# Kernel tuning notes

Measured on AMD Instinct MI355X. Metric: run time of the kernel, lower is better.

The kernel has to match this reference:

```python
import jax, jax.numpy as jnp
import numpy as np

N_NODES, N_EDGES, D_IN, N_GRAPHS = 20000, 320000, 256, 32
H1, C1, H2, C2 = 4, 128, 4, 64


def setup_inputs() -> dict:
    key = jax.random.key(0)
    ks = jax.random.split(key, 24)
    g = lambda k, shape, fan: jax.random.normal(k, shape, jnp.float32) * (1.0 / np.sqrt(fan))
    inp = {
        'x': jax.random.normal(ks[0], (N_NODES, D_IN), jnp.float32),
        'edge_index': jax.random.randint(ks[1], (2, N_EDGES), 0, N_NODES, jnp.int32),
        'batch': jnp.sort(jax.random.randint(ks[2], (N_NODES,), 0, N_GRAPHS, jnp.int32)),
        'edge_attr': jax.random.normal(ks[3], (N_EDGES, 1), jnp.float32),
        # GATConv 1: lin [D_IN, H1*C1], att_src/dst/edge [H1,C1], lin_edge [1,H1*C1], bias [H1*C1]
        'W1': g(ks[4], (D_IN, H1 * C1), D_IN),
        'as1': g(ks[5], (H1, C1), C1),
        'ad1': g(ks[6], (H1, C1), C1),
        'We1': g(ks[7], (1, H1 * C1), 1),
        'ae1': g(ks[8], (H1, C1), C1),
        'b1': jnp.zeros((H1 * C1,), jnp.float32),
        'g1': jnp.ones((H1 * C1,), jnp.float32),
        'be1': jnp.zeros((H1 * C1,), jnp.float32),
        # GATConv 2 (concat=False -> out 64)
        'W2': g(ks[9], (H1 * C1, H2 * C2), H1 * C1),
        'as2': g(ks[10], (H2, C2), C2),
        'ad2': g(ks[11], (H2, C2), C2),
        'We2': g(ks[12], (1, H2 * C2), 1),
        'ae2': g(ks[13], (H2, C2), C2),
        'b2': jnp.zeros((C2,), jnp.float32),
        'g2': jnp.ones((C2,), jnp.float32),
        'be2': jnp.zeros((C2,), jnp.float32),
        'fw1': g(ks[14], (C2, 32), C2),
        'fb1': jnp.zeros((32,), jnp.float32),
        'fw2': g(ks[15], (32, 1), 32),
        'fb2': jnp.zeros((1,), jnp.float32),
    }
    return inp


def _gat(x, src, dst, ea, W, a_s, a_d, We, a_e, bias, H, C, concat, n):
    h = (x @ W).reshape(n, H, C)                         # [N,H,C]
    al_s = jnp.einsum('nhc,hc->nh', h, a_s)              # [N,H]
    al_d = jnp.einsum('nhc,hc->nh', h, a_d)
    e = (ea @ We).reshape(-1, H, C)                      # [E',H,C]
    al_e = jnp.einsum('ehc,hc->eh', e, a_e)
    logits = jax.nn.leaky_relu(al_s[src] + al_d[dst] + al_e, 0.2)  # [E',H]
    m = jax.ops.segment_max(logits, dst, num_segments=n)
    m = jnp.where(jnp.isfinite(m), m, 0.0)
    p = jnp.exp(logits - m[dst])
    denom = jax.ops.segment_sum(p, dst, num_segments=n)
    alpha = p / (denom[dst] + 1e-16)                     # segment softmax
    out = jax.ops.segment_sum(h[src] * alpha[:, :, None], dst, num_segments=n)
    out = out.reshape(n, H * C) if concat else out.mean(axis=1)
    return out + bias


def _bn(x, gamma, beta):
    mu = x.mean(axis=0)
    var = x.var(axis=0)
    return gamma * (x - mu) * jax.lax.rsqrt(var + 1e-5) + beta


def reference(x, edge_index, batch, edge_attr, W1, as1, ad1, We1, ae1, b1, g1, be1,
              W2, as2, ad2, We2, ae2, b2, g2, be2, fw1, fb1, fw2, fb2):
    n = x.shape[0]
    loop = jnp.arange(n, dtype=edge_index.dtype)
    src = jnp.concatenate([edge_index[0], loop])
    dst = jnp.concatenate([edge_index[1], loop])
    # self-loop edge_attr filled with mean (PyG fill_value='mean')
    ea = jnp.concatenate([edge_attr, jnp.broadcast_to(edge_attr.mean(axis=0), (n, edge_attr.shape[1]))])

    h = _gat(x, src, dst, ea, W1, as1, ad1, We1, ae1, b1, H1, C1, True, n)
    h = jax.nn.elu(_bn(h, g1, be1))
    h = _gat(h, src, dst, ea, W2, as2, ad2, We2, ae2, b2, H2, C2, False, n)
    h = jax.nn.elu(_bn(h, g2, be2))

    sums = jax.ops.segment_sum(h, batch, num_segments=N_GRAPHS)
    cnt = jax.ops.segment_sum(jnp.ones((n,), h.dtype), batch, num_segments=N_GRAPHS)
    pooled = sums / jnp.maximum(cnt, 1.0)[:, None]       # global_mean_pool
    # dropout is identity in eval mode
    out = jax.nn.elu(pooled @ fw1 + fb1) @ fw2 + fb2
    return out
```

## Files before the change

kernel.cpp:

```cpp
#include <hip/hip_runtime.h>
#include <hip/hip_bf16.h>

#define N_NODES  20000
#define MPAD     20096
#define N_EDGES  320000
#define N_EP     (N_EDGES + N_NODES)
#define D_IN     256
#define N_GRAPHS 32
#define HH1 4
#define CC1 128
#define HH2 4
#define CC2 64
#define MAXDEG   128

#define XB_OFF      0ull
#define HB1_OFF     10289152ull
#define AGG1_OFF    30867456ull
#define HB2_OFF     51445760ull
#define OUT2_OFF    61734912ull
#define EAF_OFF     66854912ull
#define W1BT_OFF    68134912ull
#define W2BT_OFF    68397056ull
#define CSR_OFF     68659200ull
#define ROWPTR_OFF  71379200ull
#define GSTART_OFF  71459264ull
#define SMALL_OFF   71459520ull
#define SBUF_OFF    71485120ull
#define EAP_OFF     71485184ull
#define PMU1_OFF    72772608ull
#define PM21_OFF    73296896ull
#define PMU2_OFF    73821184ull
#define PM22_OFF    73886720ull
#define A1_OFF      73952256ull
#define B1_OFF      73954304ull
#define A2_OFF      73956352ull
#define B2_OFF      73956608ull
#define EAACC_OFF   73956864ull
#define DEG_OFF     74600000ull
#define CURS_OFF    74680000ull
#define FLAGZ_OFF   74760000ull
#define PP_OFF      74760128ull
#define ALS1_OFF    74825664ull
#define ALD1_OFF    75147200ull
#define ALS2_OFF    75468736ull
#define ALD2_OFF    75790272ull
#define ZERO0_START DEG_OFF
#define ZERO0_SIZE  1511808ull

#define S_AS1 0
#define S_AD1 512
#define S_WE1 1024
#define S_AE1 1536
#define S_G1  2048
#define S_BE1 2560
#define S_AS2 3072
#define S_AD2 3328
#define S_WE2 3584
#define S_AE2 3840
#define S_G2  4096
#define S_BE2 4160
#define S_FW1 4224
#define S_FB1 6272
#define S_FW2 6304
#define S_FB2 6336

typedef __attribute__((ext_vector_type(8))) short bf8_t;
typedef __attribute__((ext_vector_type(4))) float f4_t;

__global__ void detect_dtype(const unsigned short* __restrict__ xr, int* __restrict__ flag) {
    int i = blockIdx.x * blockDim.x + threadIdx.x;
    unsigned short u = xr[i];
    if ((u & 0x7F80) == 0x7F80) atomicOr(flag, 1);
}

__device__ __forceinline__ float loadF(const void* p, int i, int fp32) {
    return fp32 ? ((const float*)p)[i]
                : __bfloat162float(((const __hip_bfloat16*)p)[i]);
}

#define PB_XB  5024
#define PB_EAF 313
#define PB_W   512
#define PB_SM  16
#define PREP_BLOCKS (PB_XB + PB_EAF + 2 * PB_W + PB_SM + 1)
__global__ __launch_bounds__(256) void prep(
        const int* __restrict__ flag,
        const void* x, const void* ea, const void* W1, const void* W2,
        const void* as1, const void* ad1, const void* We1, const void* ae1,
        const void* g1, const void* be1, const void* as2, const void* ad2,
        const void* We2, const void* ae2, const void* g2, const void* be2,
        const void* fw1, const void* fb1, const void* fw2, const void* fb2,
        __hip_bfloat16* __restrict__ xb, float* __restrict__ eaf, float* __restrict__ eap,
        __hip_bfloat16* __restrict__ W1bt, __hip_bfloat16* __restrict__ W2bt,
        float* __restrict__ smalls, float* __restrict__ sbuf) {
    __shared__ float sh[256];
    int b = blockIdx.x, t = threadIdx.x;
    int fp32 = flag[0];
    if (b < PB_XB) {
        int base = (b * 256 + t) * 4;
        __hip_bfloat16 tmp[4];
#pragma unroll
        for (int j = 0; j < 4; ++j) {
            int i = base + j;
            float v = (i < N_NODES * D_IN) ? loadF(x, i, fp32) : 0.f;
            tmp[j] = __float2bfloat16(v);
        }
        *(uint2*)&xb[base] = *(uint2*)tmp;
        return;
    }
    b -= PB_XB;
    if (b < PB_EAF) {
        int base = (b * 256 + t) * 4;
        float s = 0.f;
#pragma unroll
        for (int j = 0; j < 4; ++j) {
            int i = base + j;
            if (i < N_EDGES) { float v = loadF(ea, i, fp32); eaf[i] = v; s += v; }
        }
        sh[t] = s;
        __syncthreads();
        for (int st = 128; st; st >>= 1) {
            if (t < st) sh[t] += sh[t + st];
            __syncthreads();
        }
        if (t == 0) eap[b] = sh[0];
        return;
    }
    b -= PB_EAF;
    if (b < PB_W) {
        int i = b * 256 + t;
        int k = i >> 9, n = i & 511;
        W1bt[(size_t)n * 256 + k] = __float2bfloat16(loadF(W1, i, fp32));
        return;
    }
    b -= PB_W;
    if (b < PB_W) {
        int i = b * 256 + t;
        int k = i >> 8, n = i & 255;
        W2bt[(size_t)n * 512 + k] = __float2bfloat16(loadF(W2, i, fp32));
        return;
    }
    b -= PB_W;
    if (b < PB_SM) {
        const void* srcs[16] = {as1, ad1, We1, ae1, g1, be1, as2, ad2, We2, ae2, g2, be2, fw1, fb1, fw2, fb2};
        const int cnts[16] = {512, 512, 512, 512, 512, 512, 256, 256, 256, 256, 64, 64, 2048, 32, 32, 1};
        const int offs[16] = {S_AS1, S_AD1, S_WE1, S_AE1, S_G1, S_BE1, S_AS2, S_AD2,
                              S_WE2, S_AE2, S_G2, S_BE2, S_FW1, S_FB1, S_FW2, S_FB2};
        for (int i = t; i < cnts[b]; i += 256)
            smalls[offs[b] + i] = loadF(srcs[b], i, fp32);
        return;
    }
    if (t < 4) {
        float s = 0.f;
        for (int c = 0; c < CC1; ++c) s += loadF(We1, t * CC1 + c, fp32) * loadF(ae1, t * CC1 + c, fp32);
        sbuf[t] = s;
    } else if (t < 8) {
        int h = t - 4;
        float s = 0.f;
        for (int c = 0; c < CC2; ++c) s += loadF(We2, h * CC2 + c, fp32) * loadF(ae2, h * CC2 + c, fp32);
        sbuf[4 + h] = s;
    }
}

#define HIST_BLOCKS 1329
__global__ void hist_bounds(const int* __restrict__ ei, int* __restrict__ deg,
                            const int* __restrict__ batch, int* __restrict__ gstart) {
    int b = blockIdx.x, t = threadIdx.x;
    if (b < HIST_BLOCKS) {
        int e = b * 256 + t;
        if (e >= N_EP) return;
        int d = (e < N_EDGES) ? ei[N_EDGES + e] : e - N_EDGES;
        atomicAdd(&deg[d], 1);
        return;
    }
    int i = (b - HIST_BLOCKS) * 256 + t;
    if (i >= N_NODES) return;
    int bb = batch[i];
    if (i == 0) {
        for (int g = 0; g <= bb; ++g) gstart[g] = 0;
    } else {
        int pb = batch[i - 1];
        for (int g = pb + 1; g <= bb; ++g) gstart[g] = i;
    }
    if (i == N_NODES - 1) {
        for (int g = bb + 1; g <= N_GRAPHS; ++g) gstart[g] = N_NODES;
    }
}

__global__ __launch_bounds__(1024) void deg_scan(const int* __restrict__ deg, int* __restrict__ rowptr,
                                                 const float* __restrict__ eap, float* __restrict__ ea_acc) {
    __shared__ int part[1024];
    __shared__ float fsh[512];
    int t = threadIdx.x;
    int lo = t * 20;
    int hi = lo + 20; if (hi > N_NODES) hi = N_NODES; if (lo > N_NODES) lo = N_NODES;
    int s = 0;
    for (int i = lo; i < hi; ++i) s += deg[i];
    part[t] = s;
    __syncthreads();
    for (int off = 1; off < 1024; off <<= 1) {
        int u = (t >= off) ? part[t - off] : 0;
        __syncthreads();
        if (t >= off) part[t] += u;
        __syncthreads();
    }
    int run = part[t] - s;
    for (int i = lo; i < hi; ++i) { rowptr[i] = run; run += deg[i]; }
    if (hi == N_NODES && lo < N_NODES) rowptr[N_NODES] = run;
    if (t < 512) fsh[t] = (t < PB_EAF) ? eap[t] : 0.f;
    __syncthreads();
    for (int st = 256; st; st >>= 1) {
        if (t < st) fsh[t] += fsh[t + st];
        __syncthreads();
    }
    if (t == 0) ea_acc[0] = fsh[0];
}

__global__ void edge_scatter(const int* __restrict__ ei, const int* __restrict__ rowptr,
                             int* __restrict__ cursor, int2* __restrict__ csr_se) {
    int e = blockIdx.x * blockDim.x + threadIdx.x;
    if (e >= N_EP) return;
    int s, d;
    if (e < N_EDGES) { s = ei[e]; d = ei[N_EDGES + e]; }
    else { s = d = e - N_EDGES; }
    int pos = rowptr[d] + atomicAdd(&cursor[d], 1);
    csr_se[pos] = make_int2(s, e);
}

__global__ __launch_bounds__(64) void csr_sort_fill(const int* __restrict__ rowptr, int2* __restrict__ cs,
                                                    const float* __restrict__ eaf,
                                                    const float* __restrict__ ea_acc) {
    __shared__ int2 buf[128];
    int d = blockIdx.x;
    int beg = rowptr[d], end = rowptr[d + 1], n = end - beg;
    int lane = threadIdx.x;
    float ea_mean = ea_acc[0] * (1.0f / N_EDGES);
    if (n <= 0) return;
    if (n <= 128) {
        for (int i = lane; i < n; i += 64) buf[i] = cs[beg + i];
        __syncthreads();
        for (int r = 0; r < n; ++r) {
            int i = 2 * lane + (r & 1);
            if (i + 1 < n) {
                int2 a = buf[i], b = buf[i + 1];
                if (a.y > b.y) { buf[i] = b; buf[i + 1] = a; }
            }
            __syncthreads();
        }
        for (int i = lane; i < n; i += 64) {
            int2 se = buf[i];
            float eav = (se.y < N_EDGES) ? eaf[se.y] : ea_mean;
            se.y = __float_as_int(eav);
            cs[beg + i] = se;
        }
    } else {
        if (lane == 0) {
            for (int i = beg + 1; i < end; ++i) {
                int2 key = cs[i]; int j = i - 1;
                while (j >= beg && cs[j].y > key.y) { cs[j + 1] = cs[j]; --j; }
                cs[j + 1] = key;
            }
        }
        __syncthreads();
        for (int i = lane; i < n; i += 64) {
            int2 se = cs[beg + i];
            float eav = (se.y < N_EDGES) ? eaf[se.y] : ea_mean;
            se.y = __float_as_int(eav);
            cs[beg + i] = se;
        }
    }
}

__global__ __launch_bounds__(256) void gemm_mfma_al(
        const short* __restrict__ A, const short* __restrict__ Bt,
        __hip_bfloat16* __restrict__ Cb, int N, int K,
        float* __restrict__ als, float* __restrict__ ald,
        const float* __restrict__ asv, const float* __restrict__ adv, int cshift) {
    __shared__ short As[128 * 40];
    __shared__ short Bs[64 * 40];
    int t = threadIdx.x;
    int wv = t >> 6, lane = t & 63, quad = lane >> 4, lr = lane & 15;
    int m0 = blockIdx.y * 128, n0 = blockIdx.x * 64;
    f4_t acc[2][4] = {};
    int ra0 = t >> 2, sa0 = t & 3;
    int ra1 = (t + 256) >> 2;
    for (int k0 = 0; k0 < K; k0 += 32) {
        *(uint4*)&As[ra0 * 40 + sa0 * 8] = *(const uint4*)&A[(size_t)(m0 + ra0) * K + k0 + sa0 * 8];
        *(uint4*)&As[ra1 * 40 + sa0 * 8] = *(const uint4*)&A[(size_t)(m0 + ra1) * K + k0 + sa0 * 8];
        *(uint4*)&Bs[ra0 * 40 + sa0 * 8] = *(const uint4*)&Bt[(size_t)(n0 + ra0) * K + k0 + sa0 * 8];
        __syncthreads();
        bf8_t a0 = *(const bf8_t*)&As[(wv * 16 + lr) * 40 + quad * 8];
        bf8_t a1 = *(const bf8_t*)&As[((wv + 4) * 16 + lr) * 40 + quad * 8];
#pragma unroll
        for (int nt = 0; nt < 4; ++nt) {
            bf8_t b = *(const bf8_t*)&Bs[(nt * 16 + lr) * 40 + quad * 8];
            acc[0][nt] = __builtin_amdgcn_mfma_f32_16x16x32_bf16(a0, b, acc[0][nt], 0, 0, 0);
            acc[1][nt] = __builtin_amdgcn_mfma_f32_16x16x32_bf16(a1, b, acc[1][nt], 0, 0, 0);
        }
        __syncthreads();
    }
#pragma unroll
    for (int si = 0; si < 2; ++si) {
        int mrow = m0 + (wv + si * 4) * 16 + quad * 4;
#pragma unroll
        for (int nt = 0; nt < 4; ++nt) {
            int col = n0 + nt * 16 + lr;
#pragma unroll
            for (int r = 0; r < 4; ++r)
                Cb[(size_t)(mrow + r) * N + col] = __float2bfloat16(acc[si][nt][r]);
        }
    }
    float asv4[4], adv4[4];
#pragma unroll
    for (int nt = 0; nt < 4; ++nt) {
        asv4[nt] = asv[n0 + nt * 16 + lr];
        adv4[nt] = adv[n0 + nt * 16 + lr];
    }
    int hsel = n0 >> cshift;
#pragma unroll
    for (int si = 0; si < 2; ++si) {
#pragma unroll
        for (int r = 0; r < 4; ++r) {
            float ps = 0.f, pd = 0.f;
#pragma unroll
            for (int nt = 0; nt < 4; ++nt) {
                ps += acc[si][nt][r] * asv4[nt];
                pd += acc[si][nt][r] * adv4[nt];
            }
#pragma unroll
            for (int m = 1; m < 16; m <<= 1) {
                ps += __shfl_xor(ps, m);
                pd += __shfl_xor(pd, m);
            }
            if (lr == 0) {
                int row = m0 + (wv + si * 4) * 16 + quad * 4 + r;
                atomicAdd(&als[row * 4 + hsel], ps);
                atomicAdd(&ald[row * 4 + hsel], pd);
            }
        }
    }
}

__global__ __launch_bounds__(256) void fused_agg1(
        const int* __restrict__ rowptr, const int2* __restrict__ cs,
        const float* __restrict__ als, const float* __restrict__ ald,
        const float* __restrict__ sbuf, const __hip_bfloat16* __restrict__ hb,
        __hip_bfloat16* __restrict__ outb) {
    __shared__ float lg[4][MAXDEG * 4];
    __shared__ int   ssrc[4][MAXDEG];
    int wv = threadIdx.x >> 6, t = threadIdx.x & 63;
    int d = blockIdx.x * 4 + wv;
    int beg = rowptr[d], n = rowptr[d + 1] - beg;
    bool fit = (n <= MAXDEG);
    float4 adv = *(const float4*)&ald[d * 4];
    float adh[4] = {adv.x, adv.y, adv.z, adv.w};
    float sb4[4] = {sbuf[0], sbuf[1], sbuf[2], sbuf[3]};
    float mx[4] = {-INFINITY, -INFINITY, -INFINITY, -INFINITY};
    for (int p = t; p < n; p += 64) {
        int2 se = cs[beg + p];
        float eav = __int_as_float(se.y);
        float4 as = *(const float4*)&als[se.x * 4];
        float l[4] = {as.x, as.y, as.z, as.w};
#pragma unroll
        for (int hh = 0; hh < 4; ++hh) {
            float v = l[hh] + adh[hh] + eav * sb4[hh];
            v = v > 0.f ? v : 0.2f * v;
            l[hh] = v;
            mx[hh] = fmaxf(mx[hh], v);
        }
        if (fit) {
            *(float4*)&lg[wv][p * 4] = make_float4(l[0], l[1], l[2], l[3]);
            ssrc[wv][p] = se.x;
        }
    }
#pragma unroll
    for (int m = 1; m < 64; m <<= 1)
#pragma unroll
        for (int hh = 0; hh < 4; ++hh)
            mx[hh] = fmaxf(mx[hh], __shfl_xor(mx[hh], m));
    asm volatile("s_waitcnt lgkmcnt(0)" ::: "memory");
    int h = t >> 4;
    float mh = mx[h];
    float a[8] = {};
    float ds = 0.f;
    const __hip_bfloat16* hrow = hb + 8 * t;
#define ACC8(rr, wt) { \
    unsigned q0 = (rr).x, q1 = (rr).y, q2 = (rr).z, q3 = (rr).w; \
    a[0] += (wt) * __uint_as_float(q0 << 16); a[1] += (wt) * __uint_as_float(q0 & 0xFFFF0000u); \
    a[2] += (wt) * __uint_as_float(q1 << 16); a[3] += (wt) * __uint_as_float(q1 & 0xFFFF0000u); \
    a[4] += (wt) * __uint_as_float(q2 << 16); a[5] += (wt) * __uint_as_float(q2 & 0xFFFF0000u); \
    a[6] += (wt) * __uint_as_float(q3 << 16); a[7] += (wt) * __uint_as_float(q3 & 0xFFFF0000u); }
    if (fit) {
        int p = 0;
        for (; p + 8 <= n; p += 8) {
            int s0 = ssrc[wv][p],     s1 = ssrc[wv][p + 1], s2 = ssrc[wv][p + 2], s3 = ssrc[wv][p + 3];
            int s4 = ssrc[wv][p + 4], s5 = ssrc[wv][p + 5], s6 = ssrc[wv][p + 6], s7 = ssrc[wv][p + 7];
            uint4 r0 = *(const uint4*)&hrow[(size_t)s0 * 512];
            uint4 r1 = *(const uint4*)&hrow[(size_t)s1 * 512];
            uint4 r2 = *(const uint4*)&hrow[(size_t)s2 * 512];
            uint4 r3 = *(const uint4*)&hrow[(size_t)s3 * 512];
            uint4 r4 = *(const uint4*)&hrow[(size_t)s4 * 512];
            uint4 r5 = *(const uint4*)&hrow[(size_t)s5 * 512];
            uint4 r6 = *(const uint4*)&hrow[(size_t)s6 * 512];
            uint4 r7 = *(const uint4*)&hrow[(size_t)s7 * 512];
            float w0 = __expf(lg[wv][p * 4 + h] - mh);
            float w1 = __expf(lg[wv][p * 4 + 4 + h] - mh);
            float w2 = __expf(lg[wv][p * 4 + 8 + h] - mh);
            float w3 = __expf(lg[wv][p * 4 + 12 + h] - mh);
            float w4 = __expf(lg[wv][p * 4 + 16 + h] - mh);
            float w5 = __expf(lg[wv][p * 4 + 20 + h] - mh);
            float w6 = __expf(lg[wv][p * 4 + 24 + h] - mh);
            float w7 = __expf(lg[wv][p * 4 + 28 + h] - mh);
            ds += ((w0 + w1) + (w2 + w3)) + ((w4 + w5) + (w6 + w7));
            ACC8(r0, w0); ACC8(r1, w1); ACC8(r2, w2); ACC8(r3, w3);
            ACC8(r4, w4); ACC8(r5, w5); ACC8(r6, w6); ACC8(r7, w7);
        }
        for (; p + 4 <= n; p += 4) {
            int s0 = ssrc[wv][p], s1 = ssrc[wv][p + 1], s2 = ssrc[wv][p + 2], s3 = ssrc[wv][p + 3];
            uint4 r0 = *(const uint4*)&hrow[(size_t)s0 * 512];
            uint4 r1 = *(const uint4*)&hrow[(size_t)s1 * 512];
            uint4 r2 = *(const uint4*)&hrow[(size_t)s2 * 512];
            uint4 r3 = *(const uint4*)&hrow[(size_t)s3 * 512];
            float w0 = __expf(lg[wv][p * 4 + h] - mh);
            float w1 = __expf(lg[wv][p * 4 + 4 + h] - mh);
            float w2 = __expf(lg[wv][p * 4 + 8 + h] - mh);
            float w3 = __expf(lg[wv][p * 4 + 12 + h] - mh);
            ds += (w0 + w1) + (w2 + w3);
            ACC8(r0, w0); ACC8(r1, w1); ACC8(r2, w2); ACC8(r3, w3);
        }
        for (; p < n; ++p) {
            int s0 = ssrc[wv][p];
            uint4 r0 = *(const uint4*)&hrow[(size_t)s0 * 512];
            float w0 = __expf(lg[wv][p * 4 + h] - mh);
            ds += w0;
            ACC8(r0, w0);
        }
    } else {
        for (int p = 0; p < n; ++p) {
            int2 se = cs[beg + p];
            float eav = __int_as_float(se.y);
            float l = als[se.x * 4 + h] + adh[h] + eav * sb4[h];
            l = l > 0.f ? l : 0.2f * l;
            float w = __expf(l - mh);
            uint4 r0 = *(const uint4*)&hrow[(size_t)se.x * 512];
            ds += w;
            ACC8(r0, w);
        }
    }
#undef ACC8
    float rdn = 1.0f / (ds + 1e-16f);
    __hip_bfloat16 tmp[8];
#pragma unroll
    for (int j = 0; j < 8; ++j) tmp[j] = __float2bfloat16(a[j] * rdn);
    *(uint4*)&outb[(size_t)d * 512 + 8 * t] = *(uint4*)tmp;
}

__global__ __launch_bounds__(256) void fused_agg2(
        const int* __restrict__ rowptr, const int2* __restrict__ cs,
        const float* __restrict__ als, const float* __restrict__ ald,
        const float* __restrict__ sbuf, const __hip_bfloat16* __restrict__ hb,
        float* __restrict__ out2) {
    __shared__ float lg[4][MAXDEG * 4];
    __shared__ int   ssrc[4][MAXDEG];
    int wv = threadIdx.x >> 6, t = threadIdx.x & 63;
    int d = blockIdx.x * 4 + wv;
    int beg = rowptr[d], n = rowptr[d + 1] - beg;
    bool fit = (n <= MAXDEG);
    float4 adv = *(const float4*)&ald[d * 4];
    float adh[4] = {adv.x, adv.y, adv.z, adv.w};
    float sb4[4] = {sbuf[4], sbuf[5], sbuf[6], sbuf[7]};
    float mx[4] = {-INFINITY, -INFINITY, -INFINITY, -INFINITY};
    for (int p = t; p < n; p += 64) {
        int2 se = cs[beg + p];
        float eav = __int_as_float(se.y);
        float4 as = *(const float4*)&als[se.x * 4];
        float l[4] = {as.x, as.y, as.z, as.w};
#pragma unroll
        for (int hh = 0; hh < 4; ++hh) {
            float v = l[hh] + adh[hh] + eav * sb4[hh];
            v = v > 0.f ? v : 0.2f * v;
            l[hh] = v;
            mx[hh] = fmaxf(mx[hh], v);
        }
        if (fit) {
            *(float4*)&lg[wv][p * 4] = make_float4(l[0], l[1], l[2], l[3]);
            ssrc[wv][p] = se.x;
        }
    }
#pragma unroll
    for (int m = 1; m < 64; m <<= 1)
#pragma unroll
        for (int hh = 0; hh < 4; ++hh)
            mx[hh] = fmaxf(mx[hh], __shfl_xor(mx[hh], m));
    asm volatile("s_waitcnt lgkmcnt(0)" ::: "memory");
    int h = t >> 4;
    float mh = mx[h];
    float a4[4] = {};
    float ds = 0.f;
    const __hip_bfloat16* hrow = hb + 4 * t;
#define ACC4(rr, wt) { \
    unsigned q0 = (rr).x, q1 = (rr).y; \
    a4[0] += (wt) * __uint_as_float(q0 << 16); a4[1] += (wt) * __uint_as_float(q0 & 0xFFFF0000u); \
    a4[2] += (wt) * __uint_as_float(q1 << 16); a4[3] += (wt) * __uint_as_float(q1 & 0xFFFF0000u); }
    if (fit) {
        int p = 0;
        for (; p + 8 <= n; p += 8) {
            int s0 = ssrc[wv][p],     s1 = ssrc[wv][p + 1], s2 = ssrc[wv][p + 2], s3 = ssrc[wv][p + 3];
            int s4 = ssrc[wv][p + 4], s5 = ssrc[wv][p + 5], s6 = ssrc[wv][p + 6], s7 = ssrc[wv][p + 7];
            uint2 r0 = *(const uint2*)&hrow[(size_t)s0 * 256];
            uint2 r1 = *(const uint2*)&hrow[(size_t)s1 * 256];
            uint2 r2 = *(const uint2*)&hrow[(size_t)s2 * 256];
            uint2 r3 = *(const uint2*)&hrow[(size_t)s3 * 256];
            uint2 r4 = *(const uint2*)&hrow[(size_t)s4 * 256];
            uint2 r5 = *(const uint2*)&hrow[(size_t)s5 * 256];
            uint2 r6 = *(const uint2*)&hrow[(size_t)s6 * 256];
            uint2 r7 = *(const uint2*)&hrow[(size_t)s7 * 256];
            float w0 = __expf(lg[wv][p * 4 + h] - mh);
            float w1 = __expf(lg[wv][p * 4 + 4 + h] - mh);
            float w2 = __expf(lg[wv][p * 4 + 8 + h] - mh);
            float w3 = __expf(lg[wv][p * 4 + 12 + h] - mh);
            float w4 = __expf(lg[wv][p * 4 + 16 + h] - mh);
            float w5 = __expf(lg[wv][p * 4 + 20 + h] - mh);
            float w6 = __expf(lg[wv][p * 4 + 24 + h] - mh);
            float w7 = __expf(lg[wv][p * 4 + 28 + h] - mh);
            ds += ((w0 + w1) + (w2 + w3)) + ((w4 + w5) + (w6 + w7));
            ACC4(r0, w0); ACC4(r1, w1); ACC4(r2, w2); ACC4(r3, w3);
            ACC4(r4, w4); ACC4(r5, w5); ACC4(r6, w6); ACC4(r7, w7);
        }
        for (; p + 4 <= n; p += 4) {
            int s0 = ssrc[wv][p], s1 = ssrc[wv][p + 1], s2 = ssrc[wv][p + 2], s3 = ssrc[wv][p + 3];
            uint2 r0 = *(const uint2*)&hrow[(size_t)s0 * 256];
            uint2 r1 = *(const uint2*)&hrow[(size_t)s1 * 256];
            uint2 r2 = *(const uint2*)&hrow[(size_t)s2 * 256];
            uint2 r3 = *(const uint2*)&hrow[(size_t)s3 * 256];
            float w0 = __expf(lg[wv][p * 4 + h] - mh);
            float w1 = __expf(lg[wv][p * 4 + 4 + h] - mh);
            float w2 = __expf(lg[wv][p * 4 + 8 + h] - mh);
            float w3 = __expf(lg[wv][p * 4 + 12 + h] - mh);
            ds += (w0 + w1) + (w2 + w3);
            ACC4(r0, w0); ACC4(r1, w1); ACC4(r2, w2); ACC4(r3, w3);
        }
        for (; p < n; ++p) {
            int s0 = ssrc[wv][p];
            uint2 r0 = *(const uint2*)&hrow[(size_t)s0 * 256];
            float w0 = __expf(lg[wv][p * 4 + h] - mh);
            ds += w0;
            ACC4(r0, w0);
        }
    } else {
        for (int p = 0; p < n; ++p) {
            int2 se = cs[beg + p];
            float eav = __int_as_float(se.y);
            float l = als[se.x * 4 + h] + adh[h] + eav * sb4[h];
            l = l > 0.f ? l : 0.2f * l;
            float w = __expf(l - mh);
            uint2 r0 = *(const uint2*)&hrow[(size_t)se.x * 256];
            ds += w;
            ACC4(r0, w);
        }
    }
#undef ACC4
    float rdn = 1.0f / (ds + 1e-16f);
#pragma unroll
    for (int j = 0; j < 4; ++j) {
        float v = a4[j] * rdn;
        v += __shfl_xor(v, 16);
        v += __shfl_xor(v, 32);
        a4[j] = v * 0.25f;
    }
    if (t < 16)
        *(float4*)&out2[(size_t)d * 64 + 4 * t] = make_float4(a4[0], a4[1], a4[2], a4[3]);
}

__global__ __launch_bounds__(256) void bn_part_b(const __hip_bfloat16* __restrict__ x,
                                                 float* __restrict__ pmu, float* __restrict__ pm2) {
    int t = threadIdx.x, b = blockIdx.x;
    float s0 = 0.f, s20 = 0.f, s1 = 0.f, s21 = 0.f;
    for (int i = b; i < N_NODES; i += gridDim.x) {
        unsigned u = *(const unsigned*)&x[(size_t)i * 512 + 2 * t];
        float v0 = __uint_as_float(u << 16);
        float v1 = __uint_as_float(u & 0xFFFF0000u);
        s0 += v0; s20 += v0 * v0; s1 += v1; s21 += v1 * v1;
    }
    pmu[b * 512 + 2 * t] = s0;     pm2[b * 512 + 2 * t] = s20;
    pmu[b * 512 + 2 * t + 1] = s1; pm2[b * 512 + 2 * t + 1] = s21;
}

__global__ void bn_reduce_affine(const float* __restrict__ pmu, const float* __restrict__ pm2,
                                 const float* __restrict__ smalls, int s_g, int s_be,
                                 float* __restrict__ a, float* __restrict__ b, int nch) {
    int c = blockIdx.x * blockDim.x + threadIdx.x;
    if (c >= nch) return;
    float s = 0.f, s2 = 0.f;
    for (int bk = 0; bk < 256; ++bk) { s += pmu[bk * nch + c]; s2 += pm2[bk * nch + c]; }
    float m = s * (1.0f / N_NODES);
    float var = s2 * (1.0f / N_NODES) - m * m;
    float aa = smalls[s_g + c] * rsqrtf(var + 1e-5f);
    a[c] = aa;
    b[c] = smalls[s_be + c] - m * aa;
}

__global__ __launch_bounds__(256) void bn_apply_elu_b16(__hip_bfloat16* __restrict__ x,
                                                        const float* __restrict__ a,
                                                        const float* __restrict__ b) {
    int q = blockIdx.x * blockDim.x + threadIdx.x;
    if (q >= N_NODES * 512 / 4) return;
    int base = q * 4;
    int j = base & 511;
    uint2 raw = *(uint2*)&x[base];
    float v[4] = {__uint_as_float(raw.x << 16), __uint_as_float(raw.x & 0xFFFF0000u),
                  __uint_as_float(raw.y << 16), __uint_as_float(raw.y & 0xFFFF0000u)};
    __hip_bfloat16 tmp[4];
#pragma unroll
    for (int k = 0; k < 4; ++k) {
        float y = a[j + k] * v[k] + b[j + k];
        y = y > 0.f ? y : expm1f(y);
        tmp[k] = __float2bfloat16(y);
    }
    *(uint2*)&x[base] = *(uint2*)tmp;
}

__global__ __launch_bounds__(256) void bn2_stats(const float* __restrict__ x,
                                                 float* __restrict__ pmu, float* __restrict__ pm2) {
    int t = threadIdx.x;
    int c = t & 63, j = t >> 6;
    float ls = 0.f, ls2 = 0.f;
    for (int nd = blockIdx.x * 4 + j; nd < N_NODES; nd += gridDim.x * 4) {
        float v = x[(size_t)nd * 64 + c];
        ls += v; ls2 += v * v;
    }
    __shared__ float shs[4][64], sh2[4][64];
    shs[j][c] = ls; sh2[j][c] = ls2;
    __syncthreads();
    if (j == 0) {
        pmu[blockIdx.x * 64 + c] = shs[0][c] + shs[1][c] + shs[2][c] + shs[3][c];
        pm2[blockIdx.x * 64 + c] = sh2[0][c] + sh2[1][c] + sh2[2][c] + sh2[3][c];
    }
}

__global__ __launch_bounds__(256) void pool_mlp(const float* __restrict__ x, const int* __restrict__ gstart,
                                                const float* __restrict__ a2, const float* __restrict__ b2,
                                                const float* __restrict__ smalls, const int* __restrict__ flag,
                                                void* __restrict__ outp) {
    int g = blockIdx.x, t = threadIdx.x;
    int c = t & 63, j = t >> 6;
    int beg = gstart[g], end = gstart[g + 1];
    float ac = a2[c], bc = b2[c];
    float s = 0.f;
    for (int i = beg + j; i < end; i += 4) {
        float y = ac * x[(size_t)i * 64 + c] + bc;
        s += (y > 0.f ? y : expm1f(y));
    }
    __shared__ float sh[4][64];
    __shared__ float pooled[64];
    __shared__ float hsh[32];
    sh[j][c] = s;
    __syncthreads();
    if (t < 64) {
        int n = end - beg;
        pooled[t] = (sh[0][t] + sh[1][t] + sh[2][t] + sh[3][t]) / fmaxf((float)n, 1.0f);
    }
    __syncthreads();
    if (t < 32) {
        float acc = smalls[S_FB1 + t];
        for (int cc = 0; cc < 64; ++cc)
            acc += pooled[cc] * smalls[S_FW1 + cc * 32 + t];
        hsh[t] = acc > 0.f ? acc : expm1f(acc);
    }
    __syncthreads();
    if (t == 0) {
        float o = smalls[S_FB2];
        for (int k = 0; k < 32; ++k) o += hsh[k] * smalls[S_FW2 + k];
        if (flag[0]) ((float*)outp)[g] = o;
        else ((__hip_bfloat16*)outp)[g] = __float2bfloat16(o);
    }
}

extern "C" void kernel_launch(void* const* d_in, const int* in_sizes, int n_in,
                              void* d_out, int out_size, void* d_ws, size_t ws_size,
                              hipStream_t stream) {
    const void* x    = d_in[0];
    const int* ei    = (const int*)d_in[1];
    const int* batch = (const int*)d_in[2];
    const void* ea   = d_in[3];
    const void* W1   = d_in[4];
    const void* as1  = d_in[5];
    const void* ad1  = d_in[6];
    const void* We1  = d_in[7];
    const void* ae1  = d_in[8];
    const void* g1   = d_in[10];
    const void* be1  = d_in[11];
    const void* W2   = d_in[12];
    const void* as2  = d_in[13];
    const void* ad2  = d_in[14];
    const void* We2  = d_in[15];
    const void* ae2  = d_in[16];
    const void* g2   = d_in[18];
    const void* be2  = d_in[19];
    const void* fw1  = d_in[20];
    const void* fb1  = d_in[21];
    const void* fw2  = d_in[22];
    const void* fb2  = d_in[23];

    char* ws = (char*)d_ws;
    __hip_bfloat16* xb   = (__hip_bfloat16*)(ws + XB_OFF);
    __hip_bfloat16* hb1  = (__hip_bfloat16*)(ws + HB1_OFF);
    __hip_bfloat16* agg1 = (__hip_bfloat16*)(ws + AGG1_OFF);
    __hip_bfloat16* hb2  = (__hip_bfloat16*)(ws + HB2_OFF);
    float* out2   = (float*)(ws + OUT2_OFF);
    float* eaf    = (float*)(ws + EAF_OFF);
    __hip_bfloat16* W1bt = (__hip_bfloat16*)(ws + W1BT_OFF);
    __hip_bfloat16* W2bt = (__hip_bfloat16*)(ws + W2BT_OFF);
    int2*  csr_se = (int2*)(ws + CSR_OFF);
    int*   rowptr = (int*)(ws + ROWPTR_OFF);
    int*   gstart = (int*)(ws + GSTART_OFF);
    float* smalls = (float*)(ws + SMALL_OFF);
    float* sbuf   = (float*)(ws + SBUF_OFF);
    float* eap    = (float*)(ws + EAP_OFF);
    float* pmu1   = (float*)(ws + PMU1_OFF);
    float* pm21   = (float*)(ws + PM21_OFF);
    float* pmu2   = (float*)(ws + PMU2_OFF);
    float* pm22   = (float*)(ws + PM22_OFF);
    float* a1     = (float*)(ws + A1_OFF);
    float* b1     = (float*)(ws + B1_OFF);
    float* a2     = (float*)(ws + A2_OFF);
    float* b2     = (float*)(ws + B2_OFF);
    float* ea_acc = (float*)(ws + EAACC_OFF);
    float* als1   = (float*)(ws + ALS1_OFF);
    float* ald1   = (float*)(ws + ALD1_OFF);
    float* als2   = (float*)(ws + ALS2_OFF);
    float* ald2   = (float*)(ws + ALD2_OFF);
    int*   deg    = (int*)(ws + DEG_OFF);
    int*   cursor = (int*)(ws + CURS_OFF);
    int*   flag   = (int*)(ws + FLAGZ_OFF);

    hipMemsetAsync(ws + ZERO0_START, 0, ZERO0_SIZE, stream);

    detect_dtype<<<256, 256, 0, stream>>>((const unsigned short*)x, flag);
    prep<<<PREP_BLOCKS, 256, 0, stream>>>(flag, x, ea, W1, W2,
                                          as1, ad1, We1, ae1, g1, be1, as2, ad2,
                                          We2, ae2, g2, be2, fw1, fb1, fw2, fb2,
                                          xb, eaf, eap, W1bt, W2bt, smalls, sbuf);

    hist_bounds<<<HIST_BLOCKS + 79, 256, 0, stream>>>(ei, deg, batch, gstart);
    deg_scan<<<1, 1024, 0, stream>>>(deg, rowptr, eap, ea_acc);
    edge_scatter<<<HIST_BLOCKS, 256, 0, stream>>>(ei, rowptr, cursor, csr_se);
    csr_sort_fill<<<N_NODES, 64, 0, stream>>>(rowptr, csr_se, eaf, ea_acc);

    gemm_mfma_al<<<dim3(512 / 64, MPAD / 128), 256, 0, stream>>>(
        (const short*)xb, (const short*)W1bt, hb1, 512, 256,
        als1, ald1, smalls + S_AS1, smalls + S_AD1, 7);
    fused_agg1<<<N_NODES / 4, 256, 0, stream>>>(rowptr, csr_se, als1, ald1, sbuf, hb1, agg1);
    bn_part_b<<<256, 256, 0, stream>>>(agg1, pmu1, pm21);
    bn_reduce_affine<<<2, 256, 0, stream>>>(pmu1, pm21, smalls, S_G1, S_BE1, a1, b1, 512);
    bn_apply_elu_b16<<<10000, 256, 0, stream>>>(agg1, a1, b1);

    gemm_mfma_al<<<dim3(256 / 64, MPAD / 128), 256, 0, stream>>>(
        (const short*)agg1, (const short*)W2bt, hb2, 256, 512,
        als2, ald2, smalls + S_AS2, smalls + S_AD2, 6);
    fused_agg2<<<N_NODES / 4, 256, 0, stream>>>(rowptr, csr_se, als2, ald2, sbuf, hb2, out2);
    bn2_stats<<<256, 256, 0, stream>>>(out2, pmu2, pm22);
    bn_reduce_affine<<<1, 64, 0, stream>>>(pmu2, pm22, smalls, S_G2, S_BE2, a2, b2, 64);

    pool_mlp<<<N_GRAPHS, 256, 0, stream>>>(out2, gstart, a2, b2, smalls, flag, d_out);
}
```

Measured before the change: 477.5 us.

## Split GAT layer-1 aggregation into alpha pass and column-sliced gather; parallelize pooling

```diff
diff --git a/kernel.cpp b/kernel.cpp
--- a/kernel.cpp
+++ b/kernel.cpp
@@ -46,6 +46,8 @@
 #define ALD2_OFF    75790272ull
 #define ZERO0_START DEG_OFF
 #define ZERO0_SIZE  1511808ull
+#define ALPHA_OFF   XB_OFF
+#define SRCS_OFF    5440000ull
 
 #define S_AS1 0
 #define S_AD1 512
@@ -341,17 +343,13 @@
     }
 }
 
-__global__ __launch_bounds__(256) void fused_agg1(
+__global__ __launch_bounds__(256) void alpha1(
         const int* __restrict__ rowptr, const int2* __restrict__ cs,
         const float* __restrict__ als, const float* __restrict__ ald,
-        const float* __restrict__ sbuf, const __hip_bfloat16* __restrict__ hb,
-        __hip_bfloat16* __restrict__ outb) {
-    __shared__ float lg[4][MAXDEG * 4];
-    __shared__ int   ssrc[4][MAXDEG];
+        const float* __restrict__ sbuf, float* __restrict__ alpha, int* __restrict__ srcs) {
     int wv = threadIdx.x >> 6, t = threadIdx.x & 63;
     int d = blockIdx.x * 4 + wv;
     int beg = rowptr[d], n = rowptr[d + 1] - beg;
-    bool fit = (n <= MAXDEG);
     float4 adv = *(const float4*)&ald[d * 4];
     float adh[4] = {adv.x, adv.y, adv.z, adv.w};
     float sb4[4] = {sbuf[0], sbuf[1], sbuf[2], sbuf[3]};
@@ -360,17 +358,12 @@
         int2 se = cs[beg + p];
         float eav = __int_as_float(se.y);
         float4 as = *(const float4*)&als[se.x * 4];
-        float l[4] = {as.x, as.y, as.z, as.w};
+        float l4[4] = {as.x, as.y, as.z, as.w};
 #pragma unroll
         for (int hh = 0; hh < 4; ++hh) {
-            float v = l[hh] + adh[hh] + eav * sb4[hh];
+            float v = l4[hh] + adh[hh] + eav * sb4[hh];
             v = v > 0.f ? v : 0.2f * v;
-            l[hh] = v;
             mx[hh] = fmaxf(mx[hh], v);
-        }
-        if (fit) {
-            *(float4*)&lg[wv][p * 4] = make_float4(l[0], l[1], l[2], l[3]);
-            ssrc[wv][p] = se.x;
         }
     }
 #pragma unroll
@@ -378,81 +371,82 @@
 #pragma unroll
         for (int hh = 0; hh < 4; ++hh)
             mx[hh] = fmaxf(mx[hh], __shfl_xor(mx[hh], m));
-    asm volatile("s_waitcnt lgkmcnt(0)" ::: "memory");
-    int h = t >> 4;
-    float mh = mx[h];
-    float a[8] = {};
-    float ds = 0.f;
-    const __hip_bfloat16* hrow = hb + 8 * t;
-#define ACC8(rr, wt) { \
-    unsigned q0 = (rr).x, q1 = (rr).y, q2 = (rr).z, q3 = (rr).w; \
-    a[0] += (wt) * __uint_as_float(q0 << 16); a[1] += (wt) * __uint_as_float(q0 & 0xFFFF0000u); \
-    a[2] += (wt) * __uint_as_float(q1 << 16); a[3] += (wt) * __uint_as_float(q1 & 0xFFFF0000u); \
-    a[4] += (wt) * __uint_as_float(q2 << 16); a[5] += (wt) * __uint_as_float(q2 & 0xFFFF0000u); \
-    a[6] += (wt) * __uint_as_float(q3 << 16); a[7] += (wt) * __uint_as_float(q3 & 0xFFFF0000u); }
-    if (fit) {
-        int p = 0;
-        for (; p + 8 <= n; p += 8) {
-            int s0 = ssrc[wv][p],     s1 = ssrc[wv][p + 1], s2 = ssrc[wv][p + 2], s3 = ssrc[wv][p + 3];
-            int s4 = ssrc[wv][p + 4], s5 = ssrc[wv][p + 5], s6 = ssrc[wv][p + 6], s7 = ssrc[wv][p + 7];
-            uint4 r0 = *(const uint4*)&hrow[(size_t)s0 * 512];
-            uint4 r1 = *(const uint4*)&hrow[(size_t)s1 * 512];
-            uint4 r2 = *(const uint4*)&hrow[(size_t)s2 * 512];
-            uint4 r3 = *(const uint4*)&hrow[(size_t)s3 * 512];
-            uint4 r4 = *(const uint4*)&hrow[(size_t)s4 * 512];
-            uint4 r5 = *(const uint4*)&hrow[(size_t)s5 * 512];
-            uint4 r6 = *(const uint4*)&hrow[(size_t)s6 * 512];
-            uint4 r7 = *(const uint4*)&hrow[(size_t)s7 * 512];
-            float w0 = __expf(lg[wv][p * 4 + h] - mh);
-            float w1 = __expf(lg[wv][p * 4 + 4 + h] - mh);
-            float w2 = __expf(lg[wv][p * 4 + 8 + h] - mh);
-            float w3 = __expf(lg[wv][p * 4 + 12 + h] - mh);
-            float w4 = __expf(lg[wv][p * 4 + 16 + h] - mh);
-            float w5 = __expf(lg[wv][p * 4 + 20 + h] - mh);
-            float w6 = __expf(lg[wv][p * 4 + 24 + h] - mh);
-            float w7 = __expf(lg[wv][p * 4 + 28 + h] - mh);
-            ds += ((w0 + w1) + (w2 + w3)) + ((w4 + w5) + (w6 + w7));
-            ACC8(r0, w0); ACC8(r1, w1); ACC8(r2, w2); ACC8(r3, w3);
-            ACC8(r4, w4); ACC8(r5, w5); ACC8(r6, w6); ACC8(r7, w7);
-        }
-        for (; p + 4 <= n; p += 4) {
-            int s0 = ssrc[wv][p], s1 = ssrc[wv][p + 1], s2 = ssrc[wv][p + 2], s3 = ssrc[wv][p + 3];
-            uint4 r0 = *(const uint4*)&hrow[(size_t)s0 * 512];
-            uint4 r1 = *(const uint4*)&hrow[(size_t)s1 * 512];
-            uint4 r2 = *(const uint4*)&hrow[(size_t)s2 * 512];
-            uint4 r3 = *(const uint4*)&hrow[(size_t)s3 * 512];
-            float w0 = __expf(lg[wv][p * 4 + h] - mh);
-            float w1 = __expf(lg[wv][p * 4 + 4 + h] - mh);
-            float w2 = __expf(lg[wv][p * 4 + 8 + h] - mh);
-            float w3 = __expf(lg[wv][p * 4 + 12 + h] - mh);
-            ds += (w0 + w1) + (w2 + w3);
-            ACC8(r0, w0); ACC8(r1, w1); ACC8(r2, w2); ACC8(r3, w3);
-        }
-        for (; p < n; ++p) {
-            int s0 = ssrc[wv][p];
-            uint4 r0 = *(const uint4*)&hrow[(size_t)s0 * 512];
-            float w0 = __expf(lg[wv][p * 4 + h] - mh);
-            ds += w0;
-            ACC8(r0, w0);
-        }
-    } else {
-        for (int p = 0; p < n; ++p) {
-            int2 se = cs[beg + p];
-            float eav = __int_as_float(se.y);
-            float l = als[se.x * 4 + h] + adh[h] + eav * sb4[h];
-            l = l > 0.f ? l : 0.2f * l;
-            float w = __expf(l - mh);
-            uint4 r0 = *(const uint4*)&hrow[(size_t)se.x * 512];
-            ds += w;
-            ACC8(r0, w);
-        }
-    }
-#undef ACC8
-    float rdn = 1.0f / (ds + 1e-16f);
-    __hip_bfloat16 tmp[8];
-#pragma unroll
-    for (int j = 0; j < 8; ++j) tmp[j] = __float2bfloat16(a[j] * rdn);
-    *(uint4*)&outb[(size_t)d * 512 + 8 * t] = *(uint4*)tmp;
+    float sm[4] = {0.f, 0.f, 0.f, 0.f};
+    for (int p = t; p < n; p += 64) {
+        int2 se = cs[beg + p];
+        float eav = __int_as_float(se.y);
+        float4 as = *(const float4*)&als[se.x * 4];
+        float l4[4] = {as.x, as.y, as.z, as.w};
+#pragma unroll
+        for (int hh = 0; hh < 4; ++hh) {
+            float v = l4[hh] + adh[hh] + eav * sb4[hh];
+            v = v > 0.f ? v : 0.2f * v;
+            sm[hh] += __expf(v - mx[hh]);
+        }
+    }
+#pragma unroll
+    for (int m = 1; m < 64; m <<= 1)
+#pragma unroll
+        for (int hh = 0; hh < 4; ++hh)
+            sm[hh] += __shfl_xor(sm[hh], m);
+    float rdn[4];
+#pragma unroll
+    for (int hh = 0; hh < 4; ++hh) rdn[hh] = 1.0f / (sm[hh] + 1e-16f);
+    for (int p = t; p < n; p += 64) {
+        int2 se = cs[beg + p];
+        float eav = __int_as_float(se.y);
+        float4 as = *(const float4*)&als[se.x * 4];
+        float l4[4] = {as.x, as.y, as.z, as.w};
+        float av[4];
+#pragma unroll
+        for (int hh = 0; hh < 4; ++hh) {
+            float v = l4[hh] + adh[hh] + eav * sb4[hh];
+            v = v > 0.f ? v : 0.2f * v;
+            av[hh] = __expf(v - mx[hh]) * rdn[hh];
+        }
+        *(float4*)&alpha[(size_t)(beg + p) * 4] = make_float4(av[0], av[1], av[2], av[3]);
+        srcs[beg + p] = se.x;
+    }
+}
+
+__global__ __launch_bounds__(256) void agg1_slice(
+        const int* __restrict__ rowptr, const int* __restrict__ srcs,
+        const float* __restrict__ alpha, const __hip_bfloat16* __restrict__ hb,
+        __hip_bfloat16* __restrict__ outb) {
+    int slice = blockIdx.x & 7;
+    int chunk = blockIdx.x >> 3;
+    int t = threadIdx.x;
+    int grp = t >> 4, lane = t & 15;
+    int d = chunk * 16 + grp;
+    int beg = rowptr[d], n = rowptr[d + 1] - beg;
+    int h0 = slice >> 1;
+    const __hip_bfloat16* hcol = hb + slice * 64 + lane * 4;
+    const float* ap = alpha + (size_t)beg * 4 + h0;
+    const int* sp = srcs + beg;
+    float a0 = 0.f, a1 = 0.f, a2 = 0.f, a3 = 0.f;
+#define ACCS(rr, wt) { \
+    a0 += (wt) * __uint_as_float((rr).x << 16); a1 += (wt) * __uint_as_float((rr).x & 0xFFFF0000u); \
+    a2 += (wt) * __uint_as_float((rr).y << 16); a3 += (wt) * __uint_as_float((rr).y & 0xFFFF0000u); }
+    int p = 0;
+    for (; p + 4 <= n; p += 4) {
+        int s0 = sp[p], s1 = sp[p + 1], s2 = sp[p + 2], s3 = sp[p + 3];
+        float w0 = ap[4 * p], w1 = ap[4 * p + 4], w2 = ap[4 * p + 8], w3 = ap[4 * p + 12];
+        uint2 r0 = *(const uint2*)&hcol[(size_t)s0 * 512];
+        uint2 r1 = *(const uint2*)&hcol[(size_t)s1 * 512];
+        uint2 r2 = *(const uint2*)&hcol[(size_t)s2 * 512];
+        uint2 r3 = *(const uint2*)&hcol[(size_t)s3 * 512];
+        ACCS(r0, w0); ACCS(r1, w1); ACCS(r2, w2); ACCS(r3, w3);
+    }
+    for (; p < n; ++p) {
+        int s0 = sp[p];
+        float w0 = ap[4 * p];
+        uint2 r0 = *(const uint2*)&hcol[(size_t)s0 * 512];
+        ACCS(r0, w0);
+    }
+#undef ACCS
+    __hip_bfloat16 tmp[4] = {__float2bfloat16(a0), __float2bfloat16(a1),
+                             __float2bfloat16(a2), __float2bfloat16(a3)};
+    *(uint2*)&outb[(size_t)d * 512 + slice * 64 + lane * 4] = *(uint2*)tmp;
 }
 
 __global__ __launch_bounds__(256) void fused_agg2(
@@ -638,28 +632,37 @@
     }
 }
 
-__global__ __launch_bounds__(256) void pool_mlp(const float* __restrict__ x, const int* __restrict__ gstart,
-                                                const float* __restrict__ a2, const float* __restrict__ b2,
-                                                const float* __restrict__ smalls, const int* __restrict__ flag,
-                                                void* __restrict__ outp) {
-    int g = blockIdx.x, t = threadIdx.x;
+__global__ __launch_bounds__(256) void pool_part(const float* __restrict__ x, const int* __restrict__ gstart,
+                                                 const float* __restrict__ a2, const float* __restrict__ b2,
+                                                 float* __restrict__ pp) {
+    int g = blockIdx.x >> 3, ck = blockIdx.x & 7;
+    int t = threadIdx.x;
     int c = t & 63, j = t >> 6;
-    int beg = gstart[g], end = gstart[g + 1];
+    int beg = gstart[g], end = gstart[g + 1], n = end - beg;
+    int cb = beg + (n * ck) / 8, ce = beg + (n * (ck + 1)) / 8;
     float ac = a2[c], bc = b2[c];
     float s = 0.f;
-    for (int i = beg + j; i < end; i += 4) {
+    for (int i = cb + j; i < ce; i += 4) {
         float y = ac * x[(size_t)i * 64 + c] + bc;
         s += (y > 0.f ? y : expm1f(y));
     }
     __shared__ float sh[4][64];
+    sh[j][c] = s;
+    __syncthreads();
+    if (j == 0)
+        pp[blockIdx.x * 64 + c] = sh[0][c] + sh[1][c] + sh[2][c] + sh[3][c];
+}
+
+__global__ __launch_bounds__(64) void pool_mlp_fin(const float* __restrict__ pp, const int* __restrict__ gstart,
+                                                   const float* __restrict__ smalls, const int* __restrict__ flag,
+                                                   void* __restrict__ outp) {
+    int g = blockIdx.x, t = threadIdx.x;
     __shared__ float pooled[64];
     __shared__ float hsh[32];
-    sh[j][c] = s;
-    __syncthreads();
-    if (t < 64) {
-        int n = end - beg;
-        pooled[t] = (sh[0][t] + sh[1][t] + sh[2][t] + sh[3][t]) / fmaxf((float)n, 1.0f);
-    }
+    float s = 0.f;
+    for (int k = 0; k < 8; ++k) s += pp[(g * 8 + k) * 64 + t];
+    int n = gstart[g + 1] - gstart[g];
+    pooled[t] = s / fmaxf((float)n, 1.0f);
     __syncthreads();
     if (t < 32) {
         float acc = smalls[S_FB1 + t];
@@ -730,6 +733,9 @@
     float* ald1   = (float*)(ws + ALD1_OFF);
     float* als2   = (float*)(ws + ALS2_OFF);
     float* ald2   = (float*)(ws + ALD2_OFF);
+    float* alpha  = (float*)(ws + ALPHA_OFF);
+    int*   srcs   = (int*)(ws + SRCS_OFF);
+    float* pp     = (float*)(ws + PP_OFF);
     int*   deg    = (int*)(ws + DEG_OFF);
     int*   cursor = (int*)(ws + CURS_OFF);
     int*   flag   = (int*)(ws + FLAGZ_OFF);
@@ -750,7 +756,8 @@
     gemm_mfma_al<<<dim3(512 / 64, MPAD / 128), 256, 0, stream>>>(
         (const short*)xb, (const short*)W1bt, hb1, 512, 256,
         als1, ald1, smalls + S_AS1, smalls + S_AD1, 7);
-    fused_agg1<<<N_NODES / 4, 256, 0, stream>>>(rowptr, csr_se, als1, ald1, sbuf, hb1, agg1);
+    alpha1<<<N_NODES / 4, 256, 0, stream>>>(rowptr, csr_se, als1, ald1, sbuf, alpha, srcs);
+    agg1_slice<<<(N_NODES / 16) * 8, 256, 0, stream>>>(rowptr, srcs, alpha, hb1, agg1);
     bn_part_b<<<256, 256, 0, stream>>>(agg1, pmu1, pm21);
     bn_reduce_affine<<<2, 256, 0, stream>>>(pmu1, pm21, smalls, S_G1, S_BE1, a1, b1, 512);
     bn_apply_elu_b16<<<10000, 256, 0, stream>>>(agg1, a1, b1);
@@ -762,5 +769,6 @@
     bn2_stats<<<256, 256, 0, stream>>>(out2, pmu2, pm22);
     bn_reduce_affine<<<1, 64, 0, stream>>>(pmu2, pm22, smalls, S_G2, S_BE2, a2, b2, 64);
 
-    pool_mlp<<<N_GRAPHS, 256, 0, stream>>>(out2, gstart, a2, b2, smalls, flag, d_out);
-}
+    pool_part<<<N_GRAPHS * 8, 256, 0, stream>>>(out2, gstart, a2, b2, pp);
+    pool_mlp_fin<<<N_GRAPHS, 64, 0, stream>>>(pp, gstart, smalls, flag, d_out);
+}
```

Result: faster. 445.1 us (-6.8%).
